# Optimization experiments

Hardware: AMD Instinct MI355X
Metric: run time of the kernel (lower is better)

The kernel has to match this reference:

```python
import jax, jax.numpy as jnp
import numpy as np

EPS = 1e-5
SLOPE = 0.2  # LeakyReLU negative slope


def _leaky(x):
    return jnp.where(x > 0, x, SLOPE * x)


def _bn(x, gamma, beta, axes):
    # training-mode batchnorm: biased variance over `axes`, channel axis kept
    mean = jnp.mean(x, axis=axes, keepdims=True)
    var = jnp.var(x, axis=axes, keepdims=True)
    return (x - mean) * jax.lax.rsqrt(var + EPS) * gamma + beta


def setup_inputs() -> dict:
    key = jax.random.key(0)
    ks = jax.random.split(key, 8)
    T, B, C, H, W, TXT = 33, 256, 512, 4, 4, 256
    std = 0.02  # normal init per weights_init
    return {
        "frames": jax.random.normal(ks[0], (T, B, C, H, W), jnp.float32),
        "sent": jax.random.normal(ks[1], (B, TXT), jnp.float32),
        # sent_map: Linear(TXT, TXT) + BN1d
        "W_lin": jax.random.normal(ks[2], (TXT, TXT), jnp.float32) * std,
        "b_lin": jnp.zeros((TXT,), jnp.float32),
        "g_bn_s": 1.0 + jax.random.normal(ks[3], (TXT,), jnp.float32) * std,
        "b_bn_s": jnp.zeros((TXT,), jnp.float32),
        # motion_map: Conv2d(512,512,1,bias=False) + BN2d
        "W_mm": jax.random.normal(ks[4], (C, C), jnp.float32) * std,
        "g_bn_m": 1.0 + jax.random.normal(ks[5], (C,), jnp.float32) * std,
        "b_bn_m": jnp.zeros((C,), jnp.float32),
        # predictor conv1: Conv2d(512+256, 512, 1, bias=False) + BN2d
        "W_p1": jax.random.normal(ks[6], (C, C + TXT), jnp.float32) * std,
        "g_bn_p": 1.0 + jax.random.normal(ks[7], (C,), jnp.float32) * std,
        "b_bn_p": jnp.zeros((C,), jnp.float32),
        # predictor conv2: Conv2d(512, 1, 4, 2, 0, bias=False); 4x4 input -> 1x1 out
        "W_p2": jax.random.normal(jax.random.fold_in(key, 99), (C, H, W), jnp.float32) * std,
    }


def reference(frames, sent, W_lin, b_lin, g_bn_s, b_bn_s,
              W_mm, g_bn_m, b_bn_m, W_p1, g_bn_p, b_bn_p, W_p2):
    # sent_map: Linear + BN1d(batch stats) + LeakyReLU
    s = sent @ W_lin.T + b_lin                      # [B, TXT]
    s = _leaky(_bn(s, g_bn_s, b_bn_s, axes=(0,)))   # [B, TXT]

    # frame differences: [T-1, B, C, H, W]
    motions = frames[1:] - frames[:-1]

    # motion_map 1x1 conv (no bias) + per-frame BN2d + LeakyReLU
    m = jnp.einsum('tbchw,oc->tbohw', motions, W_mm)
    g = g_bn_m[None, None, :, None, None]
    b = b_bn_m[None, None, :, None, None]
    m = _leaky(_bn(m, g, b, axes=(1, 3, 4)))        # BN stats per frame t, over (B,H,W)

    # broadcast sentence vector over spatial dims (replaces nested python loops)
    T, B, _, H, W = m.shape
    s_dupe = jnp.broadcast_to(s[None, :, :, None, None], (T, B, s.shape[1], H, W))
    ms = jnp.concatenate([m, s_dupe], axis=2)       # [T, B, 768, H, W]

    # predictor: 1x1 conv + per-frame BN2d + LeakyReLU
    p = jnp.einsum('tbchw,oc->tbohw', ms, W_p1)
    gp = g_bn_p[None, None, :, None, None]
    bp = b_bn_p[None, None, :, None, None]
    p = _leaky(_bn(p, gp, bp, axes=(1, 3, 4)))

    # 4x4 stride-2 valid conv on 4x4 input == full contraction -> [T, B]
    out = jax.nn.sigmoid(jnp.einsum('tbchw,chw->tb', p, W_p2))
    return out
```

## Files before the change

kernel.cpp:

```cpp
#include <hip/hip_runtime.h>
#include <hip/hip_bf16.h>

typedef __attribute__((ext_vector_type(8))) unsigned short ushort8;
typedef __attribute__((ext_vector_type(8))) short bf16x8;
typedef __attribute__((ext_vector_type(4))) float f32x4;

#define TM 32
#define NB 256
#define NC 512
#define NO 512
#define HW 16
#define TXT 256

#define SB()     __builtin_amdgcn_sched_barrier(0)
#define BAR()    __builtin_amdgcn_s_barrier()
#define PRIO1()  __builtin_amdgcn_s_setprio(1)
#define PRIO0()  __builtin_amdgcn_s_setprio(0)
#define WAITV6() asm volatile("s_waitcnt vmcnt(6) lgkmcnt(0)" ::: "memory")
#define WAITV4() asm volatile("s_waitcnt vmcnt(4) lgkmcnt(0)" ::: "memory")
#define WAITV0() asm volatile("s_waitcnt vmcnt(0) lgkmcnt(0)" ::: "memory")
#define WAITL()  asm volatile("s_waitcnt lgkmcnt(0)" ::: "memory")

__device__ __forceinline__ float bf2f(unsigned short u) {
    return __uint_as_float(((unsigned)u) << 16);
}
__device__ __forceinline__ unsigned pk2bf(float lo, float hi) {
    __hip_bfloat162 h = __float22bfloat162_rn(float2{lo, hi});
    return *reinterpret_cast<unsigned*>(&h);
}
__device__ __forceinline__ float leaky_f(float x) { return fmaxf(x, 0.2f * x); }

__device__ __forceinline__ void gl_lds16(const void* g, void* l) {
    __builtin_amdgcn_global_load_lds(
        (const __attribute__((address_space(1))) unsigned int*)g,
        (__attribute__((address_space(3))) unsigned int*)l, 16, 0, 0);
}

__global__ __launch_bounds__(256)
void kprep_w(const float* __restrict__ Wmm, const float* __restrict__ Wp1,
             const float* __restrict__ Wp2,
             unsigned short* __restrict__ WmmBf, unsigned short* __restrict__ Wp1Bf,
             float* __restrict__ Wp2T)
{
    const int bid = blockIdx.x, tid = threadIdx.x;
    if (bid < 512) {
        const float2 v = *reinterpret_cast<const float2*>(Wmm + (size_t)bid * 512 + tid * 2);
        ((unsigned*)WmmBf)[bid * 256 + tid] = pk2bf(v.x, v.y);
    } else if (bid < 1024) {
        const int o = bid - 512;
        const float2 v = *reinterpret_cast<const float2*>(Wp1 + (size_t)o * 768 + tid * 2);
        ((unsigned*)Wp1Bf)[o * 256 + tid] = pk2bf(v.x, v.y);
    } else {
        const int i = (bid - 1024) * 256 + tid;
        const int hw = i >> 9, o = i & 511;
        Wp2T[i] = Wp2[o * 16 + hw];
    }
}

__global__ __launch_bounds__(256)
void kprep_diff(const float* __restrict__ frames, unsigned short* __restrict__ mdT)
{
    __shared__ __attribute__((aligned(16))) char lds[16 * 1040];
    const int bx = blockIdx.x;
    const int tg = bx >> 8, b = bx & 255;
    const int t0 = tg * 8;
    const int tid = threadIdx.x;
    const int cb  = (tid >> 2) * 2;
    const int hw0 = (tid & 3) * 4;
    const int hw  = tid >> 4, cg = tid & 15;
    const float* fb = frames + (size_t)t0 * 2097152 + (size_t)b * 8192;

    float4 pA[4], pB[4], cA[4], cB[4];
    #pragma unroll
    for (int it = 0; it < 4; ++it) {
        const int c = cb + it * 128;
        pA[it] = *reinterpret_cast<const float4*>(fb + c * 16 + hw0);
        pB[it] = *reinterpret_cast<const float4*>(fb + (c + 1) * 16 + hw0);
    }
    #pragma unroll
    for (int dt = 0; dt < 8; ++dt) {
        const float* fc = fb + (size_t)(dt + 1) * 2097152;
        #pragma unroll
        for (int it = 0; it < 4; ++it) {
            const int c = cb + it * 128;
            cA[it] = *reinterpret_cast<const float4*>(fc + c * 16 + hw0);
            cB[it] = *reinterpret_cast<const float4*>(fc + (c + 1) * 16 + hw0);
        }
        #pragma unroll
        for (int it = 0; it < 4; ++it) {
            const int c = cb + it * 128;
            float dA[4], dB[4];
            dA[0] = cA[it].x - pA[it].x; dA[1] = cA[it].y - pA[it].y;
            dA[2] = cA[it].z - pA[it].z; dA[3] = cA[it].w - pA[it].w;
            dB[0] = cB[it].x - pB[it].x; dB[1] = cB[it].y - pB[it].y;
            dB[2] = cB[it].z - pB[it].z; dB[3] = cB[it].w - pB[it].w;
            #pragma unroll
            for (int j = 0; j < 4; ++j)
                *reinterpret_cast<unsigned*>(lds + (hw0 + j) * 1040 + c * 2) = pk2bf(dA[j], dB[j]);
        }
        __syncthreads();
        unsigned short* outp = mdT + ((size_t)((t0 + dt) * 4096 + b * 16 + hw)) * 512;
        #pragma unroll
        for (int r = 0; r < 4; ++r) {
            const int c16 = cg + r * 16;
            const uint4 v = *reinterpret_cast<const uint4*>(lds + hw * 1040 + c16 * 16);
            *reinterpret_cast<uint4*>(outp + c16 * 8) = v;
        }
        __syncthreads();
        #pragma unroll
        for (int it = 0; it < 4; ++it) { pA[it] = cA[it]; pB[it] = cB[it]; }
    }
}

__global__ __launch_bounds__(256)
void k1_sent(const float* __restrict__ sent, const float* __restrict__ W_lin,
             const float* __restrict__ b_lin, const float* __restrict__ g_bn_s,
             const float* __restrict__ b_bn_s, float* __restrict__ s_t)
{
    const int j = blockIdx.x;
    const int b = threadIdx.x;
    __shared__ float wl[TXT];
    wl[b] = W_lin[j * TXT + b];
    __syncthreads();
    float acc = b_lin[j];
    const float* srow = sent + b * TXT;
    #pragma unroll 4
    for (int k = 0; k < TXT; k += 4) {
        float4 sv = *reinterpret_cast<const float4*>(srow + k);
        acc = fmaf(sv.x, wl[k], acc);
        acc = fmaf(sv.y, wl[k+1], acc);
        acc = fmaf(sv.z, wl[k+2], acc);
        acc = fmaf(sv.w, wl[k+3], acc);
    }
    float s1 = acc, s2 = acc * acc;
    #pragma unroll
    for (int m = 1; m < 64; m <<= 1) { s1 += __shfl_xor(s1, m, 64); s2 += __shfl_xor(s2, m, 64); }
    __shared__ float r1[4], r2[4];
    if ((b & 63) == 0) { r1[b >> 6] = s1; r2[b >> 6] = s2; }
    __syncthreads();
    const float invN = 1.0f / 256.0f;
    float mean = (r1[0] + r1[1] + r1[2] + r1[3]) * invN;
    float var  = (r2[0] + r2[1] + r2[2] + r2[3]) * invN - mean * mean;
    float rstd = rsqrtf(var + 1e-5f);
    float y = (acc - mean) * rstd * g_bn_s[j] + b_bn_s[j];
    s_t[j * NB + b] = leaky_f(y);
}

__global__ __launch_bounds__(256)
void k2_sp(const float* __restrict__ s_t, const float* __restrict__ W_p1,
           float* __restrict__ sp_bt)
{
    const int o = blockIdx.x;
    const int b = threadIdx.x;
    __shared__ float wl[TXT];
    wl[b] = W_p1[o * (NC + TXT) + NC + b];
    __syncthreads();
    float acc = 0.0f;
    #pragma unroll 8
    for (int k = 0; k < TXT; ++k)
        acc = fmaf(s_t[k * NB + b], wl[k], acc);
    sp_bt[(size_t)b * NO + o] = acc;
}


__global__ __launch_bounds__(256, 3)
void k3_mfma(const unsigned short* __restrict__ WmmBf, const unsigned short* __restrict__ mdT,
             unsigned short* __restrict__ mraw,
             float* __restrict__ ssum, float* __restrict__ ssq)
{
    __shared__ __attribute__((aligned(16))) char smem[49152];
    const int bx0 = blockIdx.x;
    const int bx = (bx0 & 7) * 512 + (bx0 >> 3);
    const int ot = bx & 3, nt = (bx >> 2) & 31, t = bx >> 7;
    const int o0 = ot * 128, n0 = nt * 128;
    const int tid = threadIdx.x;
    const int w = tid >> 6, l = tid & 63;
    const int wo = w >> 1, wn = w & 1;
    const int l15 = l & 15, l16 = l >> 4;

    const char* Ag = (const char*)WmmBf + (size_t)o0 * 1024;
    const char* Bg = (const char*)mdT + ((size_t)(t * 4096 + n0)) * 1024;

    int srcOff[2], dstOff[2];
    #pragma unroll
    for (int i = 0; i < 2; ++i) {
        const int rb = (w << 5) + (i << 4);
        const int row = rb + (l >> 2);
        srcOff[i] = row * 1024 + (((l & 3) ^ ((row >> 1) & 3)) << 4);
        dstOff[i] = rb * 64;
    }

    int offA[4], offB[4];
    #pragma unroll
    for (int m = 0; m < 4; ++m) {
        const int rowA = wo * 64 + m * 16 + l15;
        const int rowB = wn * 64 + m * 16 + l15;
        offA[m] = rowA * 64 + ((l16 ^ ((rowA >> 1) & 3)) << 4);
        offB[m] = 8192 + rowB * 64 + ((l16 ^ ((rowB >> 1) & 3)) << 4);
    }

    f32x4 acc[4][4];
    #pragma unroll
    for (int i = 0; i < 4; ++i)
        #pragma unroll
        for (int j = 0; j < 4; ++j) acc[i][j] = (f32x4)0.0f;

    auto stage = [&](int kc, int buf) {
        char* dst = smem + buf * 16384;
        #pragma unroll
        for (int i = 0; i < 2; ++i)
            gl_lds16(Ag + srcOff[i] + kc * 64, dst + dstOff[i]);
        #pragma unroll
        for (int i = 0; i < 2; ++i)
            gl_lds16(Bg + srcOff[i] + kc * 64, dst + 8192 + dstOff[i]);
    };

    stage(0, 0);
    stage(1, 1);
    SB(); WAITV4(); SB(); BAR();

    #pragma unroll
    for (int kc = 0; kc < 16; ++kc) {
        const int cur = (kc % 3) * 16384;
        if (kc < 14) stage(kc + 2, (kc + 2) % 3);
        SB();
        {
            bf16x8 a[4], b[4];
            #pragma unroll
            for (int m = 0; m < 4; ++m) a[m] = *reinterpret_cast<const bf16x8*>(smem + cur + offA[m]);
            #pragma unroll
            for (int n = 0; n < 4; ++n) b[n] = *reinterpret_cast<const bf16x8*>(smem + cur + offB[n]);
            PRIO1();
            #pragma unroll
            for (int m = 0; m < 4; ++m)
                #pragma unroll
                for (int n = 0; n < 4; ++n)
                    acc[m][n] = __builtin_amdgcn_mfma_f32_16x16x32_bf16(a[m], b[n], acc[m][n], 0, 0, 0);
            PRIO0();
        }
        SB();
        if (kc < 14)       { WAITV4(); }
        else if (kc == 14) { WAITV0(); }
        else               { WAITL();  }
        SB();
        BAR();
    }

    #pragma unroll
    for (int m = 0; m < 4; ++m) {
        #pragma unroll
        for (int r = 0; r < 4; ++r) {
            float s1 = 0.0f, s2 = 0.0f;
            #pragma unroll
            for (int nn = 0; nn < 4; ++nn) {
                const float v = acc[m][nn][r];
                s1 += v; s2 = fmaf(v, v, s2);
            }
            #pragma unroll
            for (int msk = 1; msk < 16; msk <<= 1) {
                s1 += __shfl_xor(s1, msk, 64);
                s2 += __shfl_xor(s2, msk, 64);
            }
            if (l15 == 0) {
                const int o = o0 + wo * 64 + m * 16 + (l16 << 2) + r;
                atomicAdd(&ssum[t * NO + o], s1);
                atomicAdd(&ssq[t * NO + o], s2);
            }
        }
    }

    char* ep = smem;
    #pragma unroll
    for (int m = 0; m < 4; ++m) {
        #pragma unroll
        for (int nn = 0; nn < 4; ++nn) {
            uint2 u;
            u.x = pk2bf(acc[m][nn][0], acc[m][nn][1]);
            u.y = pk2bf(acc[m][nn][2], acc[m][nn][3]);
            const int row = wn * 64 + nn * 16 + l15;
            const int g   = wo * 8 + m * 2 + (l16 >> 1);
            const int off = row * 256 + ((g ^ (row & 7)) << 4) + ((l16 & 1) << 3);
            *reinterpret_cast<uint2*>(ep + off) = u;
        }
    }
    SB(); WAITL(); SB(); BAR();
    #pragma unroll
    for (int p = 0; p < 8; ++p) {
        const int row = (p << 4) + (tid >> 4);
        const int c   = tid & 15;
        const uint4 v = *reinterpret_cast<const uint4*>(ep + row * 256 + ((c ^ (row & 7)) << 4));
        *reinterpret_cast<uint4*>((char*)mraw + ((size_t)(t * 4096 + n0 + row)) * 1024
                                  + o0 * 2 + (c << 4)) = v;
    }
}

__global__ __launch_bounds__(256)
void kstats(const float* __restrict__ ssum, const float* __restrict__ ssq,
            const float* __restrict__ g, const float* __restrict__ bb,
            float* __restrict__ alpha, float* __restrict__ beta)
{
    const int i = blockIdx.x * 256 + threadIdx.x;
    const int o = i & 511;
    const float invN = 1.0f / 4096.0f;
    float mean = ssum[i] * invN;
    float var  = ssq[i] * invN - mean * mean;
    float rstd = rsqrtf(var + 1e-5f);
    float a = rstd * g[o];
    alpha[i] = a;
    beta[i]  = fmaf(-mean, a, bb[o]);
}

__global__ __launch_bounds__(256, 3)
void k5_mfma(const unsigned short* __restrict__ Wp1Bf, const unsigned short* __restrict__ mraw,
             const float* __restrict__ am, const float* __restrict__ bm,
             const float* __restrict__ sp_bt,
             unsigned short* __restrict__ praw,
             float* __restrict__ ssum, float* __restrict__ ssq)
{
    __shared__ __attribute__((aligned(16))) char smem[45056];
    float* alf = (float*)(smem + 40960);
    float* bet = (float*)(smem + 43008);
    const int bx0 = blockIdx.x;
    const int bx = (bx0 & 7) * 512 + (bx0 >> 3);
    const int ot = bx & 3, nt = (bx >> 2) & 31, t = bx >> 7;
    const int o0 = ot * 128, n0 = nt * 128;
    const int tid = threadIdx.x;
    const int w = tid >> 6, l = tid & 63;
    const int wo = w >> 1, wn = w & 1;
    const int l15 = l & 15, l16 = l >> 4;

    const char* Ag = (const char*)Wp1Bf + (size_t)o0 * 1024;

    int srcOffA[2], dstOffA[2];
    #pragma unroll
    for (int i = 0; i < 2; ++i) {
        const int rb = (w << 5) + (i << 4);
        const int row = rb + (l >> 2);
        srcOffA[i] = row * 1024 + (((l & 3) ^ ((row >> 1) & 3)) << 4);
        dstOffA[i] = rb * 64;
    }

    const int rowB_s = tid >> 1, h = tid & 1;
    const char* mrow = (const char*)mraw + ((size_t)(t * 4096 + n0 + rowB_s)) * 1024 + h * 32;
    const int bbase = rowB_s * 64;
    const int bswz = (rowB_s >> 1) & 3;

    int offA[4], offB[4];
    #pragma unroll
    for (int m = 0; m < 4; ++m) {
        const int rowA = wo * 64 + m * 16 + l15;
        const int rowB = wn * 64 + m * 16 + l15;
        offA[m] = rowA * 64 + ((l16 ^ ((rowA >> 1) & 3)) << 4);
        offB[m] = rowB * 64 + ((l16 ^ ((rowB >> 1) & 3)) << 4);
    }

    f32x4 acc[4][4];
    #pragma unroll
    for (int i = 0; i < 4; ++i)
        #pragma unroll
        for (int j = 0; j < 4; ++j) acc[i][j] = (f32x4)0.0f;

    ushort8 ur[3][2];

    auto gldsA = [&](int kc, int buf) {
        char* dst = smem + buf * 8192;
        #pragma unroll
        for (int i = 0; i < 2; ++i)
            gl_lds16(Ag + srcOffA[i] + kc * 64, dst + dstOffA[i]);
    };
    auto loadU = [&](int slot, int kc) {
        #pragma unroll
        for (int q = 0; q < 2; ++q)
            ur[slot][q] = *reinterpret_cast<const ushort8*>(mrow + kc * 64 + q * 16);
    };
    auto procB = [&](int slot, int kc, int btoff) {
        #pragma unroll
        for (int q = 0; q < 2; ++q) {
            const int kbase = kc * 32 + h * 16 + q * 8;
            float v[8];
            #pragma unroll
            for (int e = 0; e < 8; ++e)
                v[e] = leaky_f(fmaf(bf2f(ur[slot][q][e]), alf[kbase + e], bet[kbase + e]));
            uint4 pk;
            pk.x = pk2bf(v[0], v[1]);
            pk.y = pk2bf(v[2], v[3]);
            pk.z = pk2bf(v[4], v[5]);
            pk.w = pk2bf(v[6], v[7]);
            *reinterpret_cast<uint4*>(smem + btoff + bbase + ((((h << 1) + q) ^ bswz) << 4)) = pk;
        }
    };

    {
        const float* amt = am + t * NC;
        const float* bmt = bm + t * NC;
        const float2 a2 = *reinterpret_cast<const float2*>(amt + tid * 2);
        const float2 b2 = *reinterpret_cast<const float2*>(bmt + tid * 2);
        *reinterpret_cast<float2*>(alf + tid * 2) = a2;
        *reinterpret_cast<float2*>(bet + tid * 2) = b2;
    }
    loadU(0, 0);
    gldsA(0, 0);
    loadU(1, 1);
    gldsA(1, 1);
    loadU(2, 2);
    SB(); WAITL(); SB(); BAR();
    procB(0, 0, 24576);
    SB(); WAITV6(); SB(); BAR();

    #pragma unroll
    for (int kc = 0; kc < 16; ++kc) {
        const int acur = (kc % 3) * 8192;
        const int bcur = 24576 + (kc & 1) * 8192;
        if (kc < 14) gldsA(kc + 2, (kc + 2) % 3);
        SB();
        if (kc < 15) procB((kc + 1) % 3, kc + 1, 24576 + ((kc + 1) & 1) * 8192);
        if (kc < 13) loadU(kc % 3, kc + 3);
        SB();
        {
            bf16x8 a[4], b[4];
            #pragma unroll
            for (int m = 0; m < 4; ++m) a[m] = *reinterpret_cast<const bf16x8*>(smem + acur + offA[m]);
            #pragma unroll
            for (int n = 0; n < 4; ++n) b[n] = *reinterpret_cast<const bf16x8*>(smem + bcur + offB[n]);
            PRIO1();
            #pragma unroll
            for (int m = 0; m < 4; ++m)
                #pragma unroll
                for (int n = 0; n < 4; ++n)
                    acc[m][n] = __builtin_amdgcn_mfma_f32_16x16x32_bf16(a[m], b[n], acc[m][n], 0, 0, 0);
            PRIO0();
        }
        SB();
        if (kc < 13)       { WAITV6(); }
        else if (kc == 13) { WAITV4(); }
        else if (kc == 14) { WAITV0(); }
        else               { WAITL();  }
        SB();
        BAR();
    }

    char* ep = smem;
    #pragma unroll
    for (int m = 0; m < 4; ++m) {
        const int oc = o0 + wo * 64 + m * 16 + (l16 << 2);
        float s1[4] = {0,0,0,0}, s2[4] = {0,0,0,0};
        #pragma unroll
        for (int nn = 0; nn < 4; ++nn) {
            const int b = (n0 >> 4) + wn * 4 + nn;
            const float4 sp4 = *reinterpret_cast<const float4*>(sp_bt + (size_t)b * NO + oc);
            const float spv[4] = {sp4.x, sp4.y, sp4.z, sp4.w};
            float pv[4];
            #pragma unroll
            for (int r = 0; r < 4; ++r) {
                const float v = acc[m][nn][r] + spv[r];
                pv[r] = v;
                s1[r] += v; s2[r] = fmaf(v, v, s2[r]);
            }
            uint2 uu;
            uu.x = pk2bf(pv[0], pv[1]);
            uu.y = pk2bf(pv[2], pv[3]);
            const int row = wn * 64 + nn * 16 + l15;
            const int g   = wo * 8 + m * 2 + (l16 >> 1);
            const int off = row * 256 + ((g ^ (row & 7)) << 4) + ((l16 & 1) << 3);
            *reinterpret_cast<uint2*>(ep + off) = uu;
        }
        #pragma unroll
        for (int r = 0; r < 4; ++r) {
            #pragma unroll
            for (int msk = 1; msk < 16; msk <<= 1) {
                s1[r] += __shfl_xor(s1[r], msk, 64);
                s2[r] += __shfl_xor(s2[r], msk, 64);
            }
            if (l15 == 0) {
                atomicAdd(&ssum[t * NO + oc + r], s1[r]);
                atomicAdd(&ssq[t * NO + oc + r], s2[r]);
            }
        }
    }
    SB(); WAITL(); SB(); BAR();
    #pragma unroll
    for (int p = 0; p < 8; ++p) {
        const int row = (p << 4) + (tid >> 4);
        const int c   = tid & 15;
        const uint4 v = *reinterpret_cast<const uint4*>(ep + row * 256 + ((c ^ (row & 7)) << 4));
        *reinterpret_cast<uint4*>((char*)praw + ((size_t)(t * 4096 + n0 + row)) * 1024
                                  + o0 * 2 + (c << 4)) = v;
    }
}

__global__ __launch_bounds__(256)
void k7_out(const unsigned short* __restrict__ praw, const float* __restrict__ ap,
            const float* __restrict__ bp, const float* __restrict__ wp2t,
            float* __restrict__ out)
{
    const int bx = blockIdx.x;
    const int t = bx >> 8, b = bx & 255;
    const int tid = threadIdx.x;
    const int o8 = (tid & 63) * 8;
    const int hwq = tid >> 6;
    const unsigned short* pr = praw + ((size_t)(t * 256 + b)) * 8192;

    float av[8], bv[8];
    *reinterpret_cast<float4*>(av)     = *reinterpret_cast<const float4*>(ap + t * NO + o8);
    *reinterpret_cast<float4*>(av + 4) = *reinterpret_cast<const float4*>(ap + t * NO + o8 + 4);
    *reinterpret_cast<float4*>(bv)     = *reinterpret_cast<const float4*>(bp + t * NO + o8);
    *reinterpret_cast<float4*>(bv + 4) = *reinterpret_cast<const float4*>(bp + t * NO + o8 + 4);

    float acc = 0.0f;
    #pragma unroll
    for (int e = 0; e < 4; ++e) {
        const int hw = hwq + e * 4;
        const ushort8 u = *reinterpret_cast<const ushort8*>(pr + hw * 512 + o8);
        float wv[8];
        *reinterpret_cast<float4*>(wv)     = *reinterpret_cast<const float4*>(wp2t + hw * NO + o8);
        *reinterpret_cast<float4*>(wv + 4) = *reinterpret_cast<const float4*>(wp2t + hw * NO + o8 + 4);
        #pragma unroll
        for (int j = 0; j < 8; ++j) {
            const float x = leaky_f(fmaf(bf2f(u[j]), av[j], bv[j]));
            acc = fmaf(x, wv[j], acc);
        }
    }
    #pragma unroll
    for (int m = 1; m < 64; m <<= 1) acc += __shfl_xor(acc, m, 64);
    __shared__ float red[4];
    if ((tid & 63) == 0) red[tid >> 6] = acc;
    __syncthreads();
    if (tid == 0) {
        float z = red[0] + red[1] + red[2] + red[3];
        out[t * NB + b] = 1.0f / (1.0f + __expf(-z));
    }
}

extern "C" void kernel_launch(void* const* d_in, const int* in_sizes, int n_in,
                              void* d_out, int out_size, void* d_ws, size_t ws_size,
                              hipStream_t stream)
{
    const float* frames = (const float*)d_in[0];
    const float* sent   = (const float*)d_in[1];
    const float* W_lin  = (const float*)d_in[2];
    const float* b_lin  = (const float*)d_in[3];
    const float* g_bn_s = (const float*)d_in[4];
    const float* b_bn_s = (const float*)d_in[5];
    const float* W_mm   = (const float*)d_in[6];
    const float* g_bn_m = (const float*)d_in[7];
    const float* b_bn_m = (const float*)d_in[8];
    const float* W_p1   = (const float*)d_in[9];
    const float* g_bn_p = (const float*)d_in[10];
    const float* b_bn_p = (const float*)d_in[11];
    const float* W_p2   = (const float*)d_in[12];
    float* out = (float*)d_out;

    char* ws = (char*)d_ws;
    const size_t BIG = 134217728;
    unsigned short* bufA = (unsigned short*)ws;
    unsigned short* bufB = (unsigned short*)(ws + BIG);
    char* small = ws + 2 * BIG;
    float* msum = (float*)(small);
    float* msq  = (float*)(small + 65536);
    float* psum = (float*)(small + 131072);
    float* psq  = (float*)(small + 196608);
    float* am   = (float*)(small + 262144);
    float* bm   = (float*)(small + 327680);
    float* apv  = (float*)(small + 393216);
    float* bpv  = (float*)(small + 458752);
    float* s_t  = (float*)(small + 524288);
    float* sp_bt= (float*)(small + 786432);
    float* wp2t = (float*)(small + 1310720);
    unsigned short* WmmBf = (unsigned short*)(small + 1343488);
    unsigned short* Wp1Bf = (unsigned short*)(small + 1867776);

    hipMemsetAsync(small, 0, 262144, stream);
    kprep_w<<<1056, 256, 0, stream>>>(W_mm, W_p1, W_p2, WmmBf, Wp1Bf, wp2t);
    kprep_diff<<<1024, 256, 0, stream>>>(frames, bufA);
    k1_sent<<<256, 256, 0, stream>>>(sent, W_lin, b_lin, g_bn_s, b_bn_s, s_t);
    k2_sp<<<512, 256, 0, stream>>>(s_t, W_p1, sp_bt);
    k3_mfma<<<4096, 256, 0, stream>>>(WmmBf, bufA, bufB, msum, msq);
    kstats<<<64, 256, 0, stream>>>(msum, msq, g_bn_m, b_bn_m, am, bm);
    k5_mfma<<<4096, 256, 0, stream>>>(Wp1Bf, bufB, am, bm, sp_bt, bufA, psum, psq);
    kstats<<<64, 256, 0, stream>>>(psum, psq, g_bn_p, b_bn_p, apv, bpv);
    k7_out<<<8192, 256, 0, stream>>>(bufA, apv, bpv, wp2t, out);
}
```

Measured before the change: 425.6 us.

## Fuse frame differencing into motion-map MFMA GEMM B-operand staging

Removes the separate frame-difference kernel and instead has the motion GEMM load fp32 frames for t and t+1 directly, subtract, convert to bf16 and write swizzled tiles into LDS. B tiles are double-buffered through registers while A weights keep the 3-stage direct-to-LDS pipeline. This eliminates writing and re-reading the intermediate bf16 difference tensor and one launch. In exchange each block reads twice the bytes as fp32 from two frames, and the four output tiles reread the same frames, so it relies on cache hits and on hiding register-load latency.

```diff
diff --git a/kernel.cpp b/kernel.cpp
--- a/kernel.cpp
+++ b/kernel.cpp
@@ -54,61 +54,6 @@
         const int i = (bid - 1024) * 256 + tid;
         const int hw = i >> 9, o = i & 511;
         Wp2T[i] = Wp2[o * 16 + hw];
-    }
-}
-
-__global__ __launch_bounds__(256)
-void kprep_diff(const float* __restrict__ frames, unsigned short* __restrict__ mdT)
-{
-    __shared__ __attribute__((aligned(16))) char lds[16 * 1040];
-    const int bx = blockIdx.x;
-    const int tg = bx >> 8, b = bx & 255;
-    const int t0 = tg * 8;
-    const int tid = threadIdx.x;
-    const int cb  = (tid >> 2) * 2;
-    const int hw0 = (tid & 3) * 4;
-    const int hw  = tid >> 4, cg = tid & 15;
-    const float* fb = frames + (size_t)t0 * 2097152 + (size_t)b * 8192;
-
-    float4 pA[4], pB[4], cA[4], cB[4];
-    #pragma unroll
-    for (int it = 0; it < 4; ++it) {
-        const int c = cb + it * 128;
-        pA[it] = *reinterpret_cast<const float4*>(fb + c * 16 + hw0);
-        pB[it] = *reinterpret_cast<const float4*>(fb + (c + 1) * 16 + hw0);
-    }
-    #pragma unroll
-    for (int dt = 0; dt < 8; ++dt) {
-        const float* fc = fb + (size_t)(dt + 1) * 2097152;
-        #pragma unroll
-        for (int it = 0; it < 4; ++it) {
-            const int c = cb + it * 128;
-            cA[it] = *reinterpret_cast<const float4*>(fc + c * 16 + hw0);
-            cB[it] = *reinterpret_cast<const float4*>(fc + (c + 1) * 16 + hw0);
-        }
-        #pragma unroll
-        for (int it = 0; it < 4; ++it) {
-            const int c = cb + it * 128;
-            float dA[4], dB[4];
-            dA[0] = cA[it].x - pA[it].x; dA[1] = cA[it].y - pA[it].y;
-            dA[2] = cA[it].z - pA[it].z; dA[3] = cA[it].w - pA[it].w;
-            dB[0] = cB[it].x - pB[it].x; dB[1] = cB[it].y - pB[it].y;
-            dB[2] = cB[it].z - pB[it].z; dB[3] = cB[it].w - pB[it].w;
-            #pragma unroll
-            for (int j = 0; j < 4; ++j)
-                *reinterpret_cast<unsigned*>(lds + (hw0 + j) * 1040 + c * 2) = pk2bf(dA[j], dB[j]);
-        }
-        __syncthreads();
-        unsigned short* outp = mdT + ((size_t)((t0 + dt) * 4096 + b * 16 + hw)) * 512;
-        #pragma unroll
-        for (int r = 0; r < 4; ++r) {
-            const int c16 = cg + r * 16;
-            const uint4 v = *reinterpret_cast<const uint4*>(lds + hw * 1040 + c16 * 16);
-            *reinterpret_cast<uint4*>(outp + c16 * 8) = v;
-        }
-        __syncthreads();
-        #pragma unroll
-        for (int it = 0; it < 4; ++it) { pA[it] = cA[it]; pB[it] = cB[it]; }
     }
 }
 
@@ -164,31 +109,34 @@
 
 
 __global__ __launch_bounds__(256, 3)
-void k3_mfma(const unsigned short* __restrict__ WmmBf, const unsigned short* __restrict__ mdT,
-             unsigned short* __restrict__ mraw,
-             float* __restrict__ ssum, float* __restrict__ ssq)
-{
-    __shared__ __attribute__((aligned(16))) char smem[49152];
+void k3_fused(const float* __restrict__ frames, const unsigned short* __restrict__ WmmBf,
+              unsigned short* __restrict__ mraw,
+              float* __restrict__ ssum, float* __restrict__ ssq)
+{
+    __shared__ __attribute__((aligned(16))) char smem[40960];
     const int bx0 = blockIdx.x;
     const int bx = (bx0 & 7) * 512 + (bx0 >> 3);
     const int ot = bx & 3, nt = (bx >> 2) & 31, t = bx >> 7;
-    const int o0 = ot * 128, n0 = nt * 128;
+    const int o0 = ot * 128, n0 = nt * 128, b0 = nt * 8;
     const int tid = threadIdx.x;
     const int w = tid >> 6, l = tid & 63;
     const int wo = w >> 1, wn = w & 1;
     const int l15 = l & 15, l16 = l >> 4;
 
     const char* Ag = (const char*)WmmBf + (size_t)o0 * 1024;
-    const char* Bg = (const char*)mdT + ((size_t)(t * 4096 + n0)) * 1024;
-
-    int srcOff[2], dstOff[2];
+
+    int srcOffA[2], dstOffA[2];
     #pragma unroll
     for (int i = 0; i < 2; ++i) {
         const int rb = (w << 5) + (i << 4);
         const int row = rb + (l >> 2);
-        srcOff[i] = row * 1024 + (((l & 3) ^ ((row >> 1) & 3)) << 4);
-        dstOff[i] = rb * 64;
-    }
+        srcOffA[i] = row * 1024 + (((l & 3) ^ ((row >> 1) & 3)) << 4);
+        dstOffA[i] = rb * 64;
+    }
+
+    const int hwq = tid & 3, cp = (tid >> 2) & 15, bq = tid >> 6;
+    const int hw0 = hwq * 4;
+    const float* fT = frames + (size_t)t * 2097152 + (size_t)(b0 + bq) * 8192 + hw0;
 
     int offA[4], offB[4];
     #pragma unroll
@@ -196,7 +144,7 @@
         const int rowA = wo * 64 + m * 16 + l15;
         const int rowB = wn * 64 + m * 16 + l15;
         offA[m] = rowA * 64 + ((l16 ^ ((rowA >> 1) & 3)) << 4);
-        offB[m] = 8192 + rowB * 64 + ((l16 ^ ((rowB >> 1) & 3)) << 4);
+        offB[m] = rowB * 64 + ((l16 ^ ((rowB >> 1) & 3)) << 4);
     }
 
     f32x4 acc[4][4];
@@ -205,31 +153,68 @@
         #pragma unroll
         for (int j = 0; j < 4; ++j) acc[i][j] = (f32x4)0.0f;
 
-    auto stage = [&](int kc, int buf) {
-        char* dst = smem + buf * 16384;
+    float4 fr000, fr001, fr010, fr011, fr100, fr101, fr110, fr111;
+
+    auto gldsA = [&](int kc, int buf) {
+        char* dst = smem + buf * 8192;
         #pragma unroll
         for (int i = 0; i < 2; ++i)
-            gl_lds16(Ag + srcOff[i] + kc * 64, dst + dstOff[i]);
-        #pragma unroll
-        for (int i = 0; i < 2; ++i)
-            gl_lds16(Bg + srcOff[i] + kc * 64, dst + 8192 + dstOff[i]);
+            gl_lds16(Ag + srcOffA[i] + kc * 64, dst + dstOffA[i]);
     };
-
-    stage(0, 0);
-    stage(1, 1);
-    SB(); WAITV4(); SB(); BAR();
+    auto loadF = [&](int kc) {
+        const int cbase = kc * 32 + cp * 2;
+        fr000 = *reinterpret_cast<const float4*>(fT + (size_t)cbase * 16);
+        fr001 = *reinterpret_cast<const float4*>(fT + (size_t)(cbase + 1) * 16);
+        fr010 = *reinterpret_cast<const float4*>(fT + 2097152 + (size_t)cbase * 16);
+        fr011 = *reinterpret_cast<const float4*>(fT + 2097152 + (size_t)(cbase + 1) * 16);
+        fr100 = *reinterpret_cast<const float4*>(fT + 32768 + (size_t)cbase * 16);
+        fr101 = *reinterpret_cast<const float4*>(fT + 32768 + (size_t)(cbase + 1) * 16);
+        fr110 = *reinterpret_cast<const float4*>(fT + 2097152 + 32768 + (size_t)cbase * 16);
+        fr111 = *reinterpret_cast<const float4*>(fT + 2097152 + 32768 + (size_t)(cbase + 1) * 16);
+    };
+    auto procD = [&](int dstbase) {
+        const int cph = (cp >> 2), cpl = (cp & 3) << 2;
+        #pragma unroll
+        for (int u = 0; u < 2; ++u) {
+            const float4 a0 = u ? fr110 : fr010;
+            const float4 a1 = u ? fr111 : fr011;
+            const float4 c0 = u ? fr100 : fr000;
+            const float4 c1 = u ? fr101 : fr001;
+            const int rb = (bq + u * 4) * 16 + hw0;
+            unsigned pk0 = pk2bf(a0.x - c0.x, a1.x - c1.x);
+            unsigned pk1 = pk2bf(a0.y - c0.y, a1.y - c1.y);
+            unsigned pk2 = pk2bf(a0.z - c0.z, a1.z - c1.z);
+            unsigned pk3 = pk2bf(a0.w - c0.w, a1.w - c1.w);
+            *reinterpret_cast<unsigned*>(smem + dstbase + (rb + 0) * 64 + ((cph ^ (((rb + 0) >> 1) & 3)) << 4) + cpl) = pk0;
+            *reinterpret_cast<unsigned*>(smem + dstbase + (rb + 1) * 64 + ((cph ^ (((rb + 1) >> 1) & 3)) << 4) + cpl) = pk1;
+            *reinterpret_cast<unsigned*>(smem + dstbase + (rb + 2) * 64 + ((cph ^ (((rb + 2) >> 1) & 3)) << 4) + cpl) = pk2;
+            *reinterpret_cast<unsigned*>(smem + dstbase + (rb + 3) * 64 + ((cph ^ (((rb + 3) >> 1) & 3)) << 4) + cpl) = pk3;
+        }
+    };
+
+    gldsA(0, 0);
+    gldsA(1, 1);
+    loadF(0);
+    SB();
+    procD(24576);
+    loadF(1);
+    SB(); WAITL(); SB(); BAR();
 
     #pragma unroll
     for (int kc = 0; kc < 16; ++kc) {
-        const int cur = (kc % 3) * 16384;
-        if (kc < 14) stage(kc + 2, (kc + 2) % 3);
+        const int acur = (kc % 3) * 8192;
+        const int bcur = 24576 + (kc & 1) * 8192;
+        if (kc < 14) gldsA(kc + 2, (kc + 2) % 3);
+        SB();
+        if (kc < 15) procD(24576 + ((kc + 1) & 1) * 8192);
+        if (kc < 14) loadF(kc + 2);
         SB();
         {
             bf16x8 a[4], b[4];
             #pragma unroll
-            for (int m = 0; m < 4; ++m) a[m] = *reinterpret_cast<const bf16x8*>(smem + cur + offA[m]);
-            #pragma unroll
-            for (int n = 0; n < 4; ++n) b[n] = *reinterpret_cast<const bf16x8*>(smem + cur + offB[n]);
+            for (int m = 0; m < 4; ++m) a[m] = *reinterpret_cast<const bf16x8*>(smem + acur + offA[m]);
+            #pragma unroll
+            for (int n = 0; n < 4; ++n) b[n] = *reinterpret_cast<const bf16x8*>(smem + bcur + offB[n]);
             PRIO1();
             #pragma unroll
             for (int m = 0; m < 4; ++m)
@@ -239,9 +224,7 @@
             PRIO0();
         }
         SB();
-        if (kc < 14)       { WAITV4(); }
-        else if (kc == 14) { WAITV0(); }
-        else               { WAITL();  }
+        WAITL();
         SB();
         BAR();
     }
@@ -571,10 +554,9 @@
 
     hipMemsetAsync(small, 0, 262144, stream);
     kprep_w<<<1056, 256, 0, stream>>>(W_mm, W_p1, W_p2, WmmBf, Wp1Bf, wp2t);
-    kprep_diff<<<1024, 256, 0, stream>>>(frames, bufA);
     k1_sent<<<256, 256, 0, stream>>>(sent, W_lin, b_lin, g_bn_s, b_bn_s, s_t);
     k2_sp<<<512, 256, 0, stream>>>(s_t, W_p1, sp_bt);
-    k3_mfma<<<4096, 256, 0, stream>>>(WmmBf, bufA, bufB, msum, msq);
+    k3_fused<<<4096, 256, 0, stream>>>(frames, WmmBf, bufB, msum, msq);
     kstats<<<64, 256, 0, stream>>>(msum, msq, g_bn_m, b_bn_m, am, bm);
     k5_mfma<<<4096, 256, 0, stream>>>(Wp1Bf, bufB, am, bm, sp_bt, bufA, psum, psq);
     kstats<<<64, 256, 0, stream>>>(psum, psq, g_bn_p, b_bn_p, apv, bpv);
```

After: 449.9 us. 1.06x slower.
